# Optimization experiments

Hardware: AMD Instinct MI355X
Metric: run time of the kernel (lower is better)

## Reference

```python
import jax, jax.numpy as jnp
import numpy as np
from jax import lax

N, M, B = 512, 1024, 1024  # signal dim, atoms, batch (batch==m required by X = W @ Gamma)
POWER_ITER = 100
IHT_ITER = 50


def setup_inputs() -> dict:
    key = jax.random.key(0)
    k1, k2 = jax.random.split(key)
    Y = jax.random.normal(k1, (B, N), dtype=jnp.float32)
    W = jax.random.normal(k2, (N, M), dtype=jnp.float32)
    return {"Y": Y, "W": W, "K": 64}


def power_method(W):
    # 100 iterations of X <- X W^T W / ||.||; returns last pre-normalization norm
    # (approx largest eigenvalue of W^T W), matching PowerMethod in the source.
    X0 = jax.random.normal(jax.random.key(42), (1, W.shape[1]), dtype=W.dtype)

    def body(i, carry):
        X, _ = carry
        X2 = (X @ W.T) @ W          # [1, m]
        nm = jnp.linalg.norm(X2)
        return (X2 / nm, nm)

    _, nm = lax.fori_loop(0, POWER_ITER, body, (X0, jnp.asarray(1.0, W.dtype)))
    return nm


def hard_threshold_k(G, K):
    # keep entries strictly larger (in abs) than the (K+1)-th largest per row
    a = jnp.sort(jnp.abs(G), axis=1)[:, ::-1]   # descending per row
    T = a[:, K][:, None]                          # [B, 1]
    return G * (jnp.abs(G) > T).astype(G.dtype)


def reference(Y, W, K):
    # NormDict: column-normalize the dictionary
    W = W / jnp.linalg.norm(W, axis=0)
    c = power_method(W)
    eta = 1.0 / c
    Yn = jnp.linalg.norm(Y)

    # IHT sparse coding
    Gamma = hard_threshold_k(Y @ (eta * W), K)     # [B, m]
    residual = Gamma @ W.T - Y                      # [B, n]

    def step(carry, _):
        Gamma, residual = carry
        Gamma = hard_threshold_k(Gamma - eta * (residual @ W), K)
        residual = Gamma @ W.T - Y
        return (Gamma, residual), jnp.linalg.norm(residual) / Yn

    (Gamma, residual), norms = lax.scan(step, (Gamma, residual), None, length=IHT_ITER)

    X = W @ Gamma  # [n, m] @ [B, m] -> requires B == m, as in the torch source
    return X, Gamma, norms
```

## Files before the change

### kernel.cpp

```cpp
#include <hip/hip_runtime.h>


#define DEV __device__ __forceinline__

constexpr int Nd = 512;
constexpr int Md = 1024;
constexpr int Bd = 1024;
constexpr int Ksp = 64;
constexpr int IHT = 50;

DEV float wave_reduce_f(float v) {
#pragma unroll
  for (int off = 32; off > 0; off >>= 1) v += __shfl_down(v, off);
  return v;
}
DEV double wave_reduce_d(double v) {
#pragma unroll
  for (int off = 32; off > 0; off >>= 1) v += __shfl_down(v, off);
  return v;
}
DEV float rfl_f(float v) {
  return __uint_as_float(__builtin_amdgcn_readfirstlane(__float_as_uint(v)));
}

__global__ void k_zero(double* dacc) {
  int t = threadIdx.x;
  if (t < 51) dacc[t] = 0.0;
}

__global__ __launch_bounds__(256) void k_colnorm(const float* __restrict__ W,
                                                 float* __restrict__ cnorm) {
  int col = blockIdx.x * 256 + threadIdx.x;
  double ss = 0.0;
  for (int i = 0; i < Nd; ++i) {
    float w = W[(size_t)i * Md + col];
    ss = fma((double)w, (double)w, ss);
  }
  cnorm[col] = (float)sqrt(ss);
}

__global__ __launch_bounds__(256) void k_normalize(const float* __restrict__ W,
                                                   const float* __restrict__ cnorm,
                                                   float* __restrict__ Wn) {
  int idx = blockIdx.x * 256 + threadIdx.x;
  Wn[idx] = W[idx] / cnorm[idx & (Md - 1)];
}

__global__ __launch_bounds__(256) void k_yn2(const float* __restrict__ Y,
                                             double* __restrict__ dacc) {
  double s = 0.0;
  for (int i = blockIdx.x * 256 + threadIdx.x; i < Bd * Nd; i += gridDim.x * 256) {
    float y = Y[i];
    s = fma((double)y, (double)y, s);
  }
  s = wave_reduce_d(s);
  __shared__ double red[4];
  int lane = threadIdx.x & 63, wid = threadIdx.x >> 6;
  if (lane == 0) red[wid] = s;
  __syncthreads();
  if (threadIdx.x == 0) atomicAdd(&dacc[0], red[0] + red[1] + red[2] + red[3]);
}

template <int BM, int BN, int TN>
__global__ __launch_bounds__(256) void k_gemm_t(const float* __restrict__ A, int lda, int ta,
                                                const float* __restrict__ B, int ldb, int tb,
                                                float* __restrict__ C, int ldc, int Kd,
                                                float scale) {
  constexpr int AE = 32 * BM / 256;
  constexpr int BE = 32 * BN / 256;
  __shared__ __align__(16) float As[32][BM + 4];
  __shared__ __align__(16) float Bs[32][BN + 4];
  const int tid = threadIdx.x;
  const int tx = tid % (BN / TN), ty = tid / (BN / TN);
  const int m0 = blockIdx.y * BM, n0 = blockIdx.x * BN;
  float ra[AE], rb[BE];
  float acc[4][TN];
#pragma unroll
  for (int i = 0; i < 4; ++i)
#pragma unroll
    for (int j = 0; j < TN; ++j) acc[i][j] = 0.f;

  auto loadA = [&](int k0) {
    if (!ta) {
      const int c = tid & 31, r0 = tid >> 5;
#pragma unroll
      for (int i = 0; i < AE; ++i)
        ra[i] = A[(size_t)(m0 + r0 + i * 8) * lda + (k0 + c)];
    } else {
      const int r = tid % BM, c0 = tid / BM;
#pragma unroll
      for (int i = 0; i < AE; ++i)
        ra[i] = A[(size_t)(k0 + c0 + i * (256 / BM)) * lda + (m0 + r)];
    }
  };
  auto storeA = [&]() {
    if (!ta) {
      const int c = tid & 31, r0 = tid >> 5;
#pragma unroll
      for (int i = 0; i < AE; ++i) As[c][r0 + i * 8] = ra[i];
    } else {
      const int r = tid % BM, c0 = tid / BM;
#pragma unroll
      for (int i = 0; i < AE; ++i) As[c0 + i * (256 / BM)][r] = ra[i];
    }
  };
  auto loadB = [&](int k0) {
    if (!tb) {
      const int c = tid % BN, r0 = tid / BN;
#pragma unroll
      for (int i = 0; i < BE; ++i)
        rb[i] = B[(size_t)(k0 + r0 + i * (256 / BN)) * ldb + (n0 + c)];
    } else {
      const int r = tid & 31, c0 = tid >> 5;
#pragma unroll
      for (int i = 0; i < BE; ++i)
        rb[i] = B[(size_t)(n0 + c0 + i * 8) * ldb + (k0 + r)];
    }
  };
  auto storeB = [&]() {
    if (!tb) {
      const int c = tid % BN, r0 = tid / BN;
#pragma unroll
      for (int i = 0; i < BE; ++i) Bs[r0 + i * (256 / BN)][c] = rb[i];
    } else {
      const int r = tid & 31, c0 = tid >> 5;
#pragma unroll
      for (int i = 0; i < BE; ++i) Bs[r][c0 + i * 8] = rb[i];
    }
  };

  loadA(0);
  loadB(0);
  storeA();
  storeB();
  __syncthreads();
  for (int k0 = 0; k0 < Kd; k0 += 32) {
    const bool more = (k0 + 32) < Kd;
    if (more) { loadA(k0 + 32); loadB(k0 + 32); }
#pragma unroll
    for (int kk = 0; kk < 32; ++kk) {
      const float4 a4 = *(const float4*)&As[kk][ty * 4];
      const float aa[4] = {a4.x, a4.y, a4.z, a4.w};
      float bb[TN];
      if constexpr (TN == 4) {
        const float4 b4 = *(const float4*)&Bs[kk][tx * 4];
        bb[0] = b4.x; bb[1] = b4.y; bb[2] = b4.z; bb[3] = b4.w;
      } else {
        const float2 b2 = *(const float2*)&Bs[kk][tx * 2];
        bb[0] = b2.x; bb[1] = b2.y;
      }
#pragma unroll
      for (int i = 0; i < 4; ++i)
#pragma unroll
        for (int j = 0; j < TN; ++j) acc[i][j] = fmaf(aa[i], bb[j], acc[i][j]);
    }
    if (more) {
      __syncthreads();
      storeA();
      storeB();
      __syncthreads();
    }
  }
#pragma unroll
  for (int i = 0; i < 4; ++i) {
    if constexpr (TN == 4) {
      float4 o;
      o.x = acc[i][0] * scale; o.y = acc[i][1] * scale;
      o.z = acc[i][2] * scale; o.w = acc[i][3] * scale;
      *(float4*)&C[(size_t)(m0 + ty * 4 + i) * ldc + n0 + tx * 4] = o;
    } else {
      float2 o;
      o.x = acc[i][0] * scale; o.y = acc[i][1] * scale;
      *(float2*)&C[(size_t)(m0 + ty * 4 + i) * ldc + n0 + tx * 2] = o;
    }
  }
}

DEV float erfinv_xla(float x) {
  float w = -log1pf(-x * x);
  float p;
  if (w < 5.0f) {
    w = w - 2.5f;
    p = 2.81022636e-08f;
    p = fmaf(p, w, 3.43273939e-07f);
    p = fmaf(p, w, -3.5233877e-06f);
    p = fmaf(p, w, -4.39150654e-06f);
    p = fmaf(p, w, 0.00021858087f);
    p = fmaf(p, w, -0.00125372503f);
    p = fmaf(p, w, -0.00417768164f);
    p = fmaf(p, w, 0.246640727f);
    p = fmaf(p, w, 1.50140941f);
  } else {
    w = sqrtf(w) - 3.0f;
    p = -0.000200214257f;
    p = fmaf(p, w, 0.000100950558f);
    p = fmaf(p, w, 0.00134934322f);
    p = fmaf(p, w, -0.00367342844f);
    p = fmaf(p, w, 0.00573950773f);
    p = fmaf(p, w, -0.0076224613f);
    p = fmaf(p, w, 0.00943887047f);
    p = fmaf(p, w, 1.00167406f);
    p = fmaf(p, w, 2.83297682f);
  }
  return p * x;
}

#define TF_ROUND(r)                                  \
  {                                                  \
    x0 += x1;                                        \
    x1 = (x1 << (r)) | (x1 >> (32 - (r)));           \
    x1 ^= x0;                                        \
  }

__global__ void k_x0(float* __restrict__ X0) {
  unsigned i = threadIdx.x;
  unsigned x0 = i, x1 = i + 512u;
  const unsigned ks0 = 0u, ks1 = 42u, ks2 = 0x1BD11BDAu ^ 42u;
  x0 += ks0; x1 += ks1;
  TF_ROUND(13) TF_ROUND(15) TF_ROUND(26) TF_ROUND(6)  x0 += ks1; x1 += ks2 + 1u;
  TF_ROUND(17) TF_ROUND(29) TF_ROUND(16) TF_ROUND(24) x0 += ks2; x1 += ks0 + 2u;
  TF_ROUND(13) TF_ROUND(15) TF_ROUND(26) TF_ROUND(6)  x0 += ks0; x1 += ks1 + 3u;
  TF_ROUND(17) TF_ROUND(29) TF_ROUND(16) TF_ROUND(24) x0 += ks1; x1 += ks2 + 4u;
  TF_ROUND(13) TF_ROUND(15) TF_ROUND(26) TF_ROUND(6)  x0 += ks2; x1 += ks0 + 5u;
  const float lo = -0.99999994f;
  const float sqrt2 = 1.41421356237f;
  {
    float f = __uint_as_float((x0 >> 9) | 0x3f800000u) - 1.0f;
    float u = fmaxf(lo, f * 2.0f + lo);
    X0[i] = sqrt2 * erfinv_xla(u);
  }
  {
    float f = __uint_as_float((x1 >> 9) | 0x3f800000u) - 1.0f;
    float u = fmaxf(lo, f * 2.0f + lo);
    X0[i + 512] = sqrt2 * erfinv_xla(u);
  }
}

__global__ __launch_bounds__(256) void k_z0(const float* __restrict__ X0,
                                            const float* __restrict__ Wn,
                                            float* __restrict__ vout) {
  const int lane = threadIdx.x & 63, wid = threadIdx.x >> 6;
  const int row = blockIdx.x * 4 + wid;
  const float4* wr = (const float4*)(Wn + (size_t)row * Md);
  const float4* x4 = (const float4*)X0;
  float s = 0.f;
#pragma unroll
  for (int e = 0; e < 4; ++e) {
    const float4 w4 = wr[lane + e * 64];
    const float4 xx = x4[lane + e * 64];
    s = fmaf(w4.x, xx.x, s); s = fmaf(w4.y, xx.y, s);
    s = fmaf(w4.z, xx.z, s); s = fmaf(w4.w, xx.w, s);
  }
  s = wave_reduce_f(s);
  if (lane == 0) vout[row] = s;
}

__global__ __launch_bounds__(256) void k_pmv(const float* __restrict__ Mmat,
                                             const float* __restrict__ vin,
                                             float* __restrict__ vout, float scale) {
  const int lane = threadIdx.x & 63, wid = threadIdx.x >> 6;
  const int row = blockIdx.x * 4 + wid;
  const float4* mr = (const float4*)(Mmat + (size_t)row * Nd);
  const float4* v4 = (const float4*)vin;
  float s = 0.f;
#pragma unroll
  for (int e = 0; e < 2; ++e) {
    const float4 m4 = mr[lane + e * 64];
    const float4 xx = v4[lane + e * 64];
    s = fmaf(m4.x, xx.x, s); s = fmaf(m4.y, xx.y, s);
    s = fmaf(m4.z, xx.z, s); s = fmaf(m4.w, xx.w, s);
  }
  s = wave_reduce_f(s);
  if (lane == 0) vout[row] = s * scale;
}

__global__ __launch_bounds__(512) void k_pfinal(const float* __restrict__ v99,
                                                const float* __restrict__ v100,
                                                float* __restrict__ cbuf) {
  __shared__ double r99[8], r100[8];
  const int t = threadIdx.x, lane = t & 63, wid = t >> 6;
  double a = (double)v99[t]; a *= a;
  double b = (double)v100[t]; b *= b;
  a = wave_reduce_d(a);
  b = wave_reduce_d(b);
  if (lane == 0) { r99[wid] = a; r100[wid] = b; }
  __syncthreads();
  if (t == 0) {
    double n99 = 0.0, n100 = 0.0;
    for (int i = 0; i < 8; ++i) { n99 += r99[i]; n100 += r100[i]; }
    float c = (float)(8.0 * sqrt(n100 / n99));
    cbuf[0] = c;
    cbuf[1] = 1.0f / c;
  }
}

__global__ __launch_bounds__(256) void k_iht_all(
    const float* __restrict__ Q, const float* __restrict__ YW,
    const float* __restrict__ cbuf, float* __restrict__ gdense,
    double* __restrict__ normacc) {
  __shared__ float u[Md];
  __shared__ float yws[Md];
  __shared__ float sval[Ksp];
  __shared__ int sidx[Ksp];
  __shared__ unsigned histbuf[2][4][256];
  __shared__ unsigned wred[4];
  __shared__ unsigned sel_need, sel_prefix;
  __shared__ double dred[4];
  __shared__ int scnt;

  const int t = threadIdx.x;
  const int b = blockIdx.x;
  const int lane = t & 63, wv = t >> 6;
  const float eta = cbuf[1];
  const float4 yw = ((const float4*)(YW + (size_t)b * Md))[t];
  ((float4*)yws)[t] = yw;
#pragma unroll
  for (int e = 0; e < 8; ++e) ((unsigned*)histbuf)[t + e * 256] = 0u;
  const float* Qt = Q + t * 4;

  for (int it = -1; it < IHT; ++it) {
    if (it >= 0) {
      const int cnt = scnt;
      float4 p = make_float4(0.f, 0.f, 0.f, 0.f);
      int k = 0;
      for (; k + 8 <= cnt; k += 8) {
#define GROW(j)                                                        \
        const int id##j = __builtin_amdgcn_readfirstlane(sidx[k + j]); \
        const float g##j = rfl_f(sval[k + j]);                         \
        const float4 q##j = *(const float4*)(Qt + (size_t)id##j * Md);
        GROW(0) GROW(1) GROW(2) GROW(3) GROW(4) GROW(5) GROW(6) GROW(7)
#undef GROW
        p.x = fmaf(g0, q0.x, p.x); p.x = fmaf(g1, q1.x, p.x);
        p.x = fmaf(g2, q2.x, p.x); p.x = fmaf(g3, q3.x, p.x);
        p.x = fmaf(g4, q4.x, p.x); p.x = fmaf(g5, q5.x, p.x);
        p.x = fmaf(g6, q6.x, p.x); p.x = fmaf(g7, q7.x, p.x);
        p.y = fmaf(g0, q0.y, p.y); p.y = fmaf(g1, q1.y, p.y);
        p.y = fmaf(g2, q2.y, p.y); p.y = fmaf(g3, q3.y, p.y);
        p.y = fmaf(g4, q4.y, p.y); p.y = fmaf(g5, q5.y, p.y);
        p.y = fmaf(g6, q6.y, p.y); p.y = fmaf(g7, q7.y, p.y);
        p.z = fmaf(g0, q0.z, p.z); p.z = fmaf(g1, q1.z, p.z);
        p.z = fmaf(g2, q2.z, p.z); p.z = fmaf(g3, q3.z, p.z);
        p.z = fmaf(g4, q4.z, p.z); p.z = fmaf(g5, q5.z, p.z);
        p.z = fmaf(g6, q6.z, p.z); p.z = fmaf(g7, q7.z, p.z);
        p.w = fmaf(g0, q0.w, p.w); p.w = fmaf(g1, q1.w, p.w);
        p.w = fmaf(g2, q2.w, p.w); p.w = fmaf(g3, q3.w, p.w);
        p.w = fmaf(g4, q4.w, p.w); p.w = fmaf(g5, q5.w, p.w);
        p.w = fmaf(g6, q6.w, p.w); p.w = fmaf(g7, q7.w, p.w);
      }
      for (; k < cnt; ++k) {
        const int id = __builtin_amdgcn_readfirstlane(sidx[k]);
        const float g = rfl_f(sval[k]);
        const float4 q = *(const float4*)(Qt + (size_t)id * Md);
        p.x = fmaf(g, q.x, p.x); p.y = fmaf(g, q.y, p.y);
        p.z = fmaf(g, q.z, p.z); p.w = fmaf(g, q.w, p.w);
      }
      ((float4*)u)[t] = p;
      __syncthreads();
      if (it >= 1) {
        double part = 0.0;
        if (t < cnt) {
          const int id = sidx[t];
          part = (double)sval[t] * ((double)u[id] - 2.0 * (double)yws[id]);
        }
        part = wave_reduce_d(part);
        if (lane == 0) dred[wv] = part;
      }
      __syncthreads();
      if (it >= 1 && t == 0)
        atomicAdd(&normacc[it - 1], dred[0] + dred[1] + dred[2] + dred[3]);
      float4 uu;
      uu.x = -(eta * (p.x - yw.x)); uu.y = -(eta * (p.y - yw.y));
      uu.z = -(eta * (p.z - yw.z)); uu.w = -(eta * (p.w - yw.w));
      ((float4*)u)[t] = uu;
      __syncthreads();
      if (t < cnt) u[sidx[t]] += sval[t];
      __syncthreads();
    } else {
      float4 uu;
      uu.x = eta * yw.x; uu.y = eta * yw.y; uu.z = eta * yw.z; uu.w = eta * yw.w;
      ((float4*)u)[t] = uu;
      __syncthreads();
    }

    float vals[4];
    unsigned key[4];
    {
      const float4 mv = ((const float4*)u)[t];
      vals[0] = mv.x; vals[1] = mv.y; vals[2] = mv.z; vals[3] = mv.w;
#pragma unroll
      for (int e = 0; e < 4; ++e) key[e] = __float_as_uint(vals[e]) & 0x7fffffffu;
    }

    unsigned need = Ksp + 1, prefix = 0u, pmask = 0u;
#pragma unroll
    for (int pass = 3; pass >= 0; --pass) {
      const int sh = 8 * pass;
      const int pb = pass & 1;
      unsigned(*hist)[256] = histbuf[pb];
#pragma unroll
      for (int e = 0; e < 4; ++e)
        if ((key[e] & pmask) == prefix) atomicAdd(&hist[wv][(key[e] >> sh) & 255u], 1u);
      __syncthreads();
      unsigned* hz = histbuf[pb ^ 1][wv];
      hz[lane] = 0u; hz[lane + 64] = 0u; hz[lane + 128] = 0u; hz[lane + 192] = 0u;
      if (wv == 0) {
        const unsigned c0 = hist[0][lane] + hist[1][lane] + hist[2][lane] + hist[3][lane];
        const unsigned c1 = hist[0][lane + 64] + hist[1][lane + 64] + hist[2][lane + 64] + hist[3][lane + 64];
        const unsigned c2 = hist[0][lane + 128] + hist[1][lane + 128] + hist[2][lane + 128] + hist[3][lane + 128];
        const unsigned c3 = hist[0][lane + 192] + hist[1][lane + 192] + hist[2][lane + 192] + hist[3][lane + 192];
        unsigned s0 = c0, s1 = c1, s2 = c2, s3 = c3;
#pragma unroll
        for (int off = 1; off < 64; off <<= 1) {
          const unsigned y0 = __shfl_down(s0, off), y1 = __shfl_down(s1, off);
          const unsigned y2 = __shfl_down(s2, off), y3 = __shfl_down(s3, off);
          if (lane + off < 64) { s0 += y0; s1 += y1; s2 += y2; s3 += y3; }
        }
        const unsigned T1 = __builtin_amdgcn_readfirstlane(s1);
        const unsigned T2 = __builtin_amdgcn_readfirstlane(s2);
        const unsigned T3 = __builtin_amdgcn_readfirstlane(s3);
        const unsigned i0 = s0 + T1 + T2 + T3;
        const unsigned i1 = s1 + T2 + T3;
        const unsigned i2 = s2 + T3;
        const unsigned i3 = s3;
        if (i0 >= need && i0 - c0 < need) { sel_prefix = prefix | ((unsigned)lane << sh); sel_need = need - (i0 - c0); }
        if (i1 >= need && i1 - c1 < need) { sel_prefix = prefix | ((unsigned)(lane + 64) << sh); sel_need = need - (i1 - c1); }
        if (i2 >= need && i2 - c2 < need) { sel_prefix = prefix | ((unsigned)(lane + 128) << sh); sel_need = need - (i2 - c2); }
        if (i3 >= need && i3 - c3 < need) { sel_prefix = prefix | ((unsigned)(lane + 192) << sh); sel_need = need - (i3 - c3); }
      }
      __syncthreads();
      prefix = sel_prefix;
      need = sel_need;
      pmask |= (255u << sh);
    }
    const unsigned Tbits = prefix;

    unsigned keep = 0u;
    unsigned myc = 0u;
#pragma unroll
    for (int e = 0; e < 4; ++e)
      if (key[e] > Tbits) { keep |= (1u << e); ++myc; }
    unsigned x = myc;
#pragma unroll
    for (int off = 1; off < 64; off <<= 1) {
      const unsigned y = __shfl_up(x, off);
      if (lane >= off) x += y;
    }
    if (lane == 63) wred[wv] = x;
    __syncthreads();
    unsigned addlo = 0u;
    for (int w2 = 0; w2 < wv; ++w2) addlo += wred[w2];
    int base = (int)(x + addlo) - (int)myc;
#pragma unroll
    for (int e = 0; e < 4; ++e) {
      if (keep & (1u << e)) {
        sidx[base] = t * 4 + e;
        sval[base] = vals[e];
        ++base;
      }
    }
    if (t == 0) scnt = (int)(wred[0] + wred[1] + wred[2] + wred[3]);
    if (it == IHT - 1) {
      float4 g;
      g.x = (keep & 1u) ? vals[0] : 0.f;
      g.y = (keep & 2u) ? vals[1] : 0.f;
      g.z = (keep & 4u) ? vals[2] : 0.f;
      g.w = (keep & 8u) ? vals[3] : 0.f;
      ((float4*)(gdense + (size_t)b * Md))[t] = g;
    }
    __syncthreads();
  }

  const int cnt = scnt;
  if (wv == 0) {
    double part = 0.0;
    if (lane < cnt) {
      const int id = sidx[lane];
      float acc2 = 0.f;
      for (int k = 0; k < cnt; ++k)
        acc2 = fmaf(sval[k], Q[(size_t)sidx[k] * Md + id], acc2);
      part = (double)sval[lane] * ((double)acc2 - 2.0 * (double)yws[id]);
    }
    part = wave_reduce_d(part);
    if (lane == 0) atomicAdd(&normacc[IHT - 1], part);
  }
}

__global__ void k_wnorms(const double* __restrict__ dacc, float* __restrict__ onorms) {
  const int t = threadIdx.x;
  if (t < IHT) {
    const double yn2 = dacc[0];
    double r2 = yn2 + dacc[1 + t];
    if (r2 < 0.0) r2 = 0.0;
    onorms[t] = (float)(sqrt(r2) / sqrt(yn2));
  }
}

extern "C" void kernel_launch(void* const* d_in, const int* in_sizes, int n_in,
                              void* d_out, int out_size, void* d_ws, size_t ws_size,
                              hipStream_t stream) {
  (void)in_sizes; (void)n_in; (void)out_size; (void)ws_size;
  const float* Y = (const float*)d_in[0];
  const float* W = (const float*)d_in[1];
  float* out = (float*)d_out;
  float* outX = out;
  float* outG = out + Nd * Md;
  float* outN = outG + Bd * Md;

  char* wsb = (char*)d_ws;
  double* dacc = (double*)wsb;
  float* cbuf = (float*)(wsb + 512);
  float* Wn = (float*)(wsb + 1024);
  float* Q = Wn + Nd * Md;
  float* YW = Q + Md * Md;
  float* Smat = YW + Bd * Md;
  float* S2 = Smat + Nd * Nd;
  float* cnorm = S2 + Nd * Nd;
  float* X0 = cnorm + Md;
  float* V = X0 + Md;

  k_zero<<<1, 64, 0, stream>>>(dacc);
  k_colnorm<<<4, 256, 0, stream>>>(W, cnorm);
  k_normalize<<<2048, 256, 0, stream>>>(W, cnorm, Wn);

  k_gemm_t<64, 32, 2><<<dim3(16, 8), 256, 0, stream>>>(Wn, Md, 0, Wn, Md, 1, Smat, Nd, Md, 1.0f);
  k_gemm_t<64, 32, 2><<<dim3(16, 8), 256, 0, stream>>>(Smat, Nd, 0, Smat, Nd, 0, S2, Nd, Nd, 0.015625f);
  k_gemm_t<64, 64, 4><<<dim3(16, 16), 256, 0, stream>>>(Wn, Md, 1, Wn, Md, 0, Q, Md, Nd, 1.0f);
  k_gemm_t<64, 64, 4><<<dim3(16, 16), 256, 0, stream>>>(Y, Nd, 0, Wn, Md, 0, YW, Md, Nd, 1.0f);
  k_yn2<<<128, 256, 0, stream>>>(Y, dacc);

  k_x0<<<1, 512, 0, stream>>>(X0);
  k_z0<<<128, 256, 0, stream>>>(X0, Wn, V);
  float* pin = V;
  float* pout = V + 512;
  for (int i = 0; i < 49; ++i) {
    k_pmv<<<128, 256, 0, stream>>>(S2, pin, pout, 1.0f);
    float* tp = pin; pin = pout; pout = tp;
  }
  k_pmv<<<128, 256, 0, stream>>>(Smat, pin, V + 1024, 0.125f);
  k_pmv<<<128, 256, 0, stream>>>(Smat, V + 1024, V + 1536, 0.125f);
  k_pfinal<<<1, 512, 0, stream>>>(V + 1024, V + 1536, cbuf);

  k_iht_all<<<1024, 256, 0, stream>>>(Q, YW, cbuf, outG, dacc + 1);
  k_wnorms<<<1, 64, 0, stream>>>(dacc, outN);

  k_gemm_t<64, 32, 2><<<dim3(32, 8), 256, 0, stream>>>(Wn, Md, 0, outG, Md, 0, outX, Md, Md, 1.0f);
}
```

Baseline: 978.2 us.

## Run IHT kernel with one wavefront per batch row instead of four

Shrinks each IHT block from 256 threads to a single 64-lane wavefront. Each lane now handles 16 coefficients, so cross-wave shared-memory reductions, per-wave histograms and most block barriers go away, and the final norm step uses the whole block. The cost is less parallelism per row, more registers per lane, and more histogram atomics per lane contending on one shared histogram. With 1024 blocks of one wave each, occupancy now depends on how many blocks fit per CU rather than on block size.

```diff
diff --git a/kernel.cpp b/kernel.cpp
--- a/kernel.cpp
+++ b/kernel.cpp
@@ -294,7 +294,7 @@
   }
 }
 
-__global__ __launch_bounds__(256) void k_iht_all(
+__global__ __launch_bounds__(64) void k_iht_all(
     const float* __restrict__ Q, const float* __restrict__ YW,
     const float* __restrict__ cbuf, float* __restrict__ gdense,
     double* __restrict__ normacc) {
@@ -302,59 +302,71 @@
   __shared__ float yws[Md];
   __shared__ float sval[Ksp];
   __shared__ int sidx[Ksp];
-  __shared__ unsigned histbuf[2][4][256];
-  __shared__ unsigned wred[4];
+  __shared__ unsigned histbuf[2][256];
   __shared__ unsigned sel_need, sel_prefix;
-  __shared__ double dred[4];
   __shared__ int scnt;
 
   const int t = threadIdx.x;
   const int b = blockIdx.x;
-  const int lane = t & 63, wv = t >> 6;
   const float eta = cbuf[1];
-  const float4 yw = ((const float4*)(YW + (size_t)b * Md))[t];
-  ((float4*)yws)[t] = yw;
-#pragma unroll
-  for (int e = 0; e < 8; ++e) ((unsigned*)histbuf)[t + e * 256] = 0u;
+  const float4* YW4 = (const float4*)(YW + (size_t)b * Md);
+  float4 yw[4], p[4];
+#pragma unroll
+  for (int j = 0; j < 4; ++j) {
+    yw[j] = YW4[j * 64 + t];
+    ((float4*)yws)[j * 64 + t] = yw[j];
+  }
+  histbuf[0][t] = 0u; histbuf[0][t + 64] = 0u; histbuf[0][t + 128] = 0u; histbuf[0][t + 192] = 0u;
+  histbuf[1][t] = 0u; histbuf[1][t + 64] = 0u; histbuf[1][t + 128] = 0u; histbuf[1][t + 192] = 0u;
   const float* Qt = Q + t * 4;
 
   for (int it = -1; it < IHT; ++it) {
+    float vals[16];
+    unsigned key[16];
     if (it >= 0) {
       const int cnt = scnt;
-      float4 p = make_float4(0.f, 0.f, 0.f, 0.f);
+#pragma unroll
+      for (int j = 0; j < 4; ++j) p[j] = make_float4(0.f, 0.f, 0.f, 0.f);
       int k = 0;
-      for (; k + 8 <= cnt; k += 8) {
-#define GROW(j)                                                        \
-        const int id##j = __builtin_amdgcn_readfirstlane(sidx[k + j]); \
-        const float g##j = rfl_f(sval[k + j]);                         \
-        const float4 q##j = *(const float4*)(Qt + (size_t)id##j * Md);
-        GROW(0) GROW(1) GROW(2) GROW(3) GROW(4) GROW(5) GROW(6) GROW(7)
-#undef GROW
-        p.x = fmaf(g0, q0.x, p.x); p.x = fmaf(g1, q1.x, p.x);
-        p.x = fmaf(g2, q2.x, p.x); p.x = fmaf(g3, q3.x, p.x);
-        p.x = fmaf(g4, q4.x, p.x); p.x = fmaf(g5, q5.x, p.x);
-        p.x = fmaf(g6, q6.x, p.x); p.x = fmaf(g7, q7.x, p.x);
-        p.y = fmaf(g0, q0.y, p.y); p.y = fmaf(g1, q1.y, p.y);
-        p.y = fmaf(g2, q2.y, p.y); p.y = fmaf(g3, q3.y, p.y);
-        p.y = fmaf(g4, q4.y, p.y); p.y = fmaf(g5, q5.y, p.y);
-        p.y = fmaf(g6, q6.y, p.y); p.y = fmaf(g7, q7.y, p.y);
-        p.z = fmaf(g0, q0.z, p.z); p.z = fmaf(g1, q1.z, p.z);
-        p.z = fmaf(g2, q2.z, p.z); p.z = fmaf(g3, q3.z, p.z);
-        p.z = fmaf(g4, q4.z, p.z); p.z = fmaf(g5, q5.z, p.z);
-        p.z = fmaf(g6, q6.z, p.z); p.z = fmaf(g7, q7.z, p.z);
-        p.w = fmaf(g0, q0.w, p.w); p.w = fmaf(g1, q1.w, p.w);
-        p.w = fmaf(g2, q2.w, p.w); p.w = fmaf(g3, q3.w, p.w);
-        p.w = fmaf(g4, q4.w, p.w); p.w = fmaf(g5, q5.w, p.w);
-        p.w = fmaf(g6, q6.w, p.w); p.w = fmaf(g7, q7.w, p.w);
+      for (; k + 4 <= cnt; k += 4) {
+        const int i0 = __builtin_amdgcn_readfirstlane(sidx[k]);
+        const int i1 = __builtin_amdgcn_readfirstlane(sidx[k + 1]);
+        const int i2 = __builtin_amdgcn_readfirstlane(sidx[k + 2]);
+        const int i3 = __builtin_amdgcn_readfirstlane(sidx[k + 3]);
+        const float g0 = rfl_f(sval[k]), g1 = rfl_f(sval[k + 1]);
+        const float g2 = rfl_f(sval[k + 2]), g3 = rfl_f(sval[k + 3]);
+        float4 q0[4], q1[4], q2[4], q3[4];
+#pragma unroll
+        for (int j = 0; j < 4; ++j) {
+          q0[j] = *(const float4*)(Qt + (size_t)i0 * Md + j * 256);
+          q1[j] = *(const float4*)(Qt + (size_t)i1 * Md + j * 256);
+          q2[j] = *(const float4*)(Qt + (size_t)i2 * Md + j * 256);
+          q3[j] = *(const float4*)(Qt + (size_t)i3 * Md + j * 256);
+        }
+#pragma unroll
+        for (int j = 0; j < 4; ++j) {
+          p[j].x = fmaf(g0, q0[j].x, p[j].x); p[j].x = fmaf(g1, q1[j].x, p[j].x);
+          p[j].x = fmaf(g2, q2[j].x, p[j].x); p[j].x = fmaf(g3, q3[j].x, p[j].x);
+          p[j].y = fmaf(g0, q0[j].y, p[j].y); p[j].y = fmaf(g1, q1[j].y, p[j].y);
+          p[j].y = fmaf(g2, q2[j].y, p[j].y); p[j].y = fmaf(g3, q3[j].y, p[j].y);
+          p[j].z = fmaf(g0, q0[j].z, p[j].z); p[j].z = fmaf(g1, q1[j].z, p[j].z);
+          p[j].z = fmaf(g2, q2[j].z, p[j].z); p[j].z = fmaf(g3, q3[j].z, p[j].z);
+          p[j].w = fmaf(g0, q0[j].w, p[j].w); p[j].w = fmaf(g1, q1[j].w, p[j].w);
+          p[j].w = fmaf(g2, q2[j].w, p[j].w); p[j].w = fmaf(g3, q3[j].w, p[j].w);
+        }
       }
       for (; k < cnt; ++k) {
         const int id = __builtin_amdgcn_readfirstlane(sidx[k]);
         const float g = rfl_f(sval[k]);
-        const float4 q = *(const float4*)(Qt + (size_t)id * Md);
-        p.x = fmaf(g, q.x, p.x); p.y = fmaf(g, q.y, p.y);
-        p.z = fmaf(g, q.z, p.z); p.w = fmaf(g, q.w, p.w);
-      }
-      ((float4*)u)[t] = p;
+#pragma unroll
+        for (int j = 0; j < 4; ++j) {
+          const float4 q = *(const float4*)(Qt + (size_t)id * Md + j * 256);
+          p[j].x = fmaf(g, q.x, p[j].x); p[j].y = fmaf(g, q.y, p[j].y);
+          p[j].z = fmaf(g, q.z, p[j].z); p[j].w = fmaf(g, q.w, p[j].w);
+        }
+      }
+#pragma unroll
+      for (int j = 0; j < 4; ++j) ((float4*)u)[j * 64 + t] = p[j];
       __syncthreads();
       if (it >= 1) {
         double part = 0.0;
@@ -363,70 +375,67 @@
           part = (double)sval[t] * ((double)u[id] - 2.0 * (double)yws[id]);
         }
         part = wave_reduce_d(part);
-        if (lane == 0) dred[wv] = part;
-      }
-      __syncthreads();
-      if (it >= 1 && t == 0)
-        atomicAdd(&normacc[it - 1], dred[0] + dred[1] + dred[2] + dred[3]);
-      float4 uu;
-      uu.x = -(eta * (p.x - yw.x)); uu.y = -(eta * (p.y - yw.y));
-      uu.z = -(eta * (p.z - yw.z)); uu.w = -(eta * (p.w - yw.w));
-      ((float4*)u)[t] = uu;
+        if (t == 0) atomicAdd(&normacc[it - 1], part);
+      }
+      __syncthreads();
+#pragma unroll
+      for (int j = 0; j < 4; ++j) {
+        float4 uu;
+        uu.x = -(eta * (p[j].x - yw[j].x)); uu.y = -(eta * (p[j].y - yw[j].y));
+        uu.z = -(eta * (p[j].z - yw[j].z)); uu.w = -(eta * (p[j].w - yw[j].w));
+        ((float4*)u)[j * 64 + t] = uu;
+      }
       __syncthreads();
       if (t < cnt) u[sidx[t]] += sval[t];
       __syncthreads();
+#pragma unroll
+      for (int j = 0; j < 4; ++j) {
+        const float4 mv = ((const float4*)u)[j * 64 + t];
+        vals[j * 4 + 0] = mv.x; vals[j * 4 + 1] = mv.y;
+        vals[j * 4 + 2] = mv.z; vals[j * 4 + 3] = mv.w;
+      }
     } else {
-      float4 uu;
-      uu.x = eta * yw.x; uu.y = eta * yw.y; uu.z = eta * yw.z; uu.w = eta * yw.w;
-      ((float4*)u)[t] = uu;
-      __syncthreads();
-    }
-
-    float vals[4];
-    unsigned key[4];
-    {
-      const float4 mv = ((const float4*)u)[t];
-      vals[0] = mv.x; vals[1] = mv.y; vals[2] = mv.z; vals[3] = mv.w;
-#pragma unroll
-      for (int e = 0; e < 4; ++e) key[e] = __float_as_uint(vals[e]) & 0x7fffffffu;
-    }
+#pragma unroll
+      for (int j = 0; j < 4; ++j) {
+        vals[j * 4 + 0] = eta * yw[j].x; vals[j * 4 + 1] = eta * yw[j].y;
+        vals[j * 4 + 2] = eta * yw[j].z; vals[j * 4 + 3] = eta * yw[j].w;
+      }
+    }
+#pragma unroll
+    for (int e = 0; e < 16; ++e) key[e] = __float_as_uint(vals[e]) & 0x7fffffffu;
 
     unsigned need = Ksp + 1, prefix = 0u, pmask = 0u;
 #pragma unroll
     for (int pass = 3; pass >= 0; --pass) {
       const int sh = 8 * pass;
       const int pb = pass & 1;
-      unsigned(*hist)[256] = histbuf[pb];
-#pragma unroll
-      for (int e = 0; e < 4; ++e)
-        if ((key[e] & pmask) == prefix) atomicAdd(&hist[wv][(key[e] >> sh) & 255u], 1u);
-      __syncthreads();
-      unsigned* hz = histbuf[pb ^ 1][wv];
-      hz[lane] = 0u; hz[lane + 64] = 0u; hz[lane + 128] = 0u; hz[lane + 192] = 0u;
-      if (wv == 0) {
-        const unsigned c0 = hist[0][lane] + hist[1][lane] + hist[2][lane] + hist[3][lane];
-        const unsigned c1 = hist[0][lane + 64] + hist[1][lane + 64] + hist[2][lane + 64] + hist[3][lane + 64];
-        const unsigned c2 = hist[0][lane + 128] + hist[1][lane + 128] + hist[2][lane + 128] + hist[3][lane + 128];
-        const unsigned c3 = hist[0][lane + 192] + hist[1][lane + 192] + hist[2][lane + 192] + hist[3][lane + 192];
-        unsigned s0 = c0, s1 = c1, s2 = c2, s3 = c3;
-#pragma unroll
-        for (int off = 1; off < 64; off <<= 1) {
-          const unsigned y0 = __shfl_down(s0, off), y1 = __shfl_down(s1, off);
-          const unsigned y2 = __shfl_down(s2, off), y3 = __shfl_down(s3, off);
-          if (lane + off < 64) { s0 += y0; s1 += y1; s2 += y2; s3 += y3; }
-        }
-        const unsigned T1 = __builtin_amdgcn_readfirstlane(s1);
-        const unsigned T2 = __builtin_amdgcn_readfirstlane(s2);
-        const unsigned T3 = __builtin_amdgcn_readfirstlane(s3);
-        const unsigned i0 = s0 + T1 + T2 + T3;
-        const unsigned i1 = s1 + T2 + T3;
-        const unsigned i2 = s2 + T3;
-        const unsigned i3 = s3;
-        if (i0 >= need && i0 - c0 < need) { sel_prefix = prefix | ((unsigned)lane << sh); sel_need = need - (i0 - c0); }
-        if (i1 >= need && i1 - c1 < need) { sel_prefix = prefix | ((unsigned)(lane + 64) << sh); sel_need = need - (i1 - c1); }
-        if (i2 >= need && i2 - c2 < need) { sel_prefix = prefix | ((unsigned)(lane + 128) << sh); sel_need = need - (i2 - c2); }
-        if (i3 >= need && i3 - c3 < need) { sel_prefix = prefix | ((unsigned)(lane + 192) << sh); sel_need = need - (i3 - c3); }
-      }
+      unsigned* hist = histbuf[pb];
+#pragma unroll
+      for (int e = 0; e < 16; ++e)
+        if ((key[e] & pmask) == prefix) atomicAdd(&hist[(key[e] >> sh) & 255u], 1u);
+      __syncthreads();
+      unsigned* hz = histbuf[pb ^ 1];
+      hz[t] = 0u; hz[t + 64] = 0u; hz[t + 128] = 0u; hz[t + 192] = 0u;
+      const unsigned c0 = hist[t], c1 = hist[t + 64];
+      const unsigned c2 = hist[t + 128], c3 = hist[t + 192];
+      unsigned s0 = c0, s1 = c1, s2 = c2, s3 = c3;
+#pragma unroll
+      for (int off = 1; off < 64; off <<= 1) {
+        const unsigned y0 = __shfl_down(s0, off), y1 = __shfl_down(s1, off);
+        const unsigned y2 = __shfl_down(s2, off), y3 = __shfl_down(s3, off);
+        if (t + off < 64) { s0 += y0; s1 += y1; s2 += y2; s3 += y3; }
+      }
+      const unsigned T1 = __builtin_amdgcn_readfirstlane(s1);
+      const unsigned T2 = __builtin_amdgcn_readfirstlane(s2);
+      const unsigned T3 = __builtin_amdgcn_readfirstlane(s3);
+      const unsigned i0 = s0 + T1 + T2 + T3;
+      const unsigned i1 = s1 + T2 + T3;
+      const unsigned i2 = s2 + T3;
+      const unsigned i3 = s3;
+      if (i0 >= need && i0 - c0 < need) { sel_prefix = prefix | ((unsigned)t << sh); sel_need = need - (i0 - c0); }
+      if (i1 >= need && i1 - c1 < need) { sel_prefix = prefix | ((unsigned)(t + 64) << sh); sel_need = need - (i1 - c1); }
+      if (i2 >= need && i2 - c2 < need) { sel_prefix = prefix | ((unsigned)(t + 128) << sh); sel_need = need - (i2 - c2); }
+      if (i3 >= need && i3 - c3 < need) { sel_prefix = prefix | ((unsigned)(t + 192) << sh); sel_need = need - (i3 - c3); }
       __syncthreads();
       prefix = sel_prefix;
       need = sel_need;
@@ -435,54 +444,67 @@
     const unsigned Tbits = prefix;
 
     unsigned keep = 0u;
-    unsigned myc = 0u;
-#pragma unroll
-    for (int e = 0; e < 4; ++e)
-      if (key[e] > Tbits) { keep |= (1u << e); ++myc; }
-    unsigned x = myc;
-#pragma unroll
-    for (int off = 1; off < 64; off <<= 1) {
-      const unsigned y = __shfl_up(x, off);
-      if (lane >= off) x += y;
-    }
-    if (lane == 63) wred[wv] = x;
+    int mycj[4];
+#pragma unroll
+    for (int j = 0; j < 4; ++j) {
+      int c = 0;
+#pragma unroll
+      for (int e = 0; e < 4; ++e)
+        if (key[j * 4 + e] > Tbits) { keep |= (1u << (j * 4 + e)); ++c; }
+      mycj[j] = c;
+    }
+    int basej[4];
+    int total = 0;
+#pragma unroll
+    for (int j = 0; j < 4; ++j) {
+      int x = mycj[j];
+#pragma unroll
+      for (int off = 1; off < 64; off <<= 1) {
+        const int y = __shfl_up(x, off);
+        if (t >= off) x += y;
+      }
+      basej[j] = total + x - mycj[j];
+      total += __shfl(x, 63);
+    }
+#pragma unroll
+    for (int j = 0; j < 4; ++j) {
+      int base = basej[j];
+#pragma unroll
+      for (int e = 0; e < 4; ++e) {
+        if (keep & (1u << (j * 4 + e))) {
+          sidx[base] = j * 256 + 4 * t + e;
+          sval[base] = vals[j * 4 + e];
+          ++base;
+        }
+      }
+    }
+    if (t == 0) scnt = total;
+    if (it == IHT - 1) {
+      float4* G4 = (float4*)(gdense + (size_t)b * Md);
+#pragma unroll
+      for (int j = 0; j < 4; ++j) {
+        float4 g;
+        g.x = (keep & (1u << (j * 4 + 0))) ? vals[j * 4 + 0] : 0.f;
+        g.y = (keep & (1u << (j * 4 + 1))) ? vals[j * 4 + 1] : 0.f;
+        g.z = (keep & (1u << (j * 4 + 2))) ? vals[j * 4 + 2] : 0.f;
+        g.w = (keep & (1u << (j * 4 + 3))) ? vals[j * 4 + 3] : 0.f;
+        G4[j * 64 + t] = g;
+      }
+    }
     __syncthreads();
-    unsigned addlo = 0u;
-    for (int w2 = 0; w2 < wv; ++w2) addlo += wred[w2];
-    int base = (int)(x + addlo) - (int)myc;
-#pragma unroll
-    for (int e = 0; e < 4; ++e) {
-      if (keep & (1u << e)) {
-        sidx[base] = t * 4 + e;
-        sval[base] = vals[e];
-        ++base;
-      }
-    }
-    if (t == 0) scnt = (int)(wred[0] + wred[1] + wred[2] + wred[3]);
-    if (it == IHT - 1) {
-      float4 g;
-      g.x = (keep & 1u) ? vals[0] : 0.f;
-      g.y = (keep & 2u) ? vals[1] : 0.f;
-      g.z = (keep & 4u) ? vals[2] : 0.f;
-      g.w = (keep & 8u) ? vals[3] : 0.f;
-      ((float4*)(gdense + (size_t)b * Md))[t] = g;
-    }
-    __syncthreads();
   }
 
   const int cnt = scnt;
-  if (wv == 0) {
-    double part = 0.0;
-    if (lane < cnt) {
-      const int id = sidx[lane];
-      float acc2 = 0.f;
-      for (int k = 0; k < cnt; ++k)
-        acc2 = fmaf(sval[k], Q[(size_t)sidx[k] * Md + id], acc2);
-      part = (double)sval[lane] * ((double)acc2 - 2.0 * (double)yws[id]);
-    }
-    part = wave_reduce_d(part);
-    if (lane == 0) atomicAdd(&normacc[IHT - 1], part);
-  }
+  double part = 0.0;
+  if (t < cnt) {
+    const int id = sidx[t];
+    float acc2 = 0.f;
+    for (int k = 0; k < cnt; ++k)
+      acc2 = fmaf(sval[k], Q[(size_t)sidx[k] * Md + id], acc2);
+    part = (double)sval[t] * ((double)acc2 - 2.0 * (double)yws[id]);
+  }
+  part = wave_reduce_d(part);
+  if (t == 0) atomicAdd(&normacc[IHT - 1], part);
 }
 
 __global__ void k_wnorms(const double* __restrict__ dacc, float* __restrict__ onorms) {
@@ -540,7 +562,7 @@
   k_pmv<<<128, 256, 0, stream>>>(Smat, V + 1024, V + 1536, 0.125f);
   k_pfinal<<<1, 512, 0, stream>>>(V + 1024, V + 1536, cbuf);
 
-  k_iht_all<<<1024, 256, 0, stream>>>(Q, YW, cbuf, outG, dacc + 1);
+  k_iht_all<<<1024, 64, 0, stream>>>(Q, YW, cbuf, outG, dacc + 1);
   k_wnorms<<<1, 64, 0, stream>>>(dacc, outN);
 
   k_gemm_t<64, 32, 2><<<dim3(32, 8), 256, 0, stream>>>(Wn, Md, 0, outG, Md, 0, outX, Md, Md, 1.0f);
```

After: 1.204 ms. +23.0%, slower.

## Fuse power-method launches into one persistent kernel with grid barriers

Applied to the files above, without the earlier changes.

Replaces the ~54 small launches of the power method (x0 generation, z0, 51 matvecs, final norm) with a single 8-block persistent kernel. The blocks synchronise between matvec steps through per-step atomic counters in global memory, which are zeroed by k_zero. This removes per-launch overhead and gaps between dependent tiny kernels, but only 8 workgroups do the matvecs and the spin barriers add latency. The IHT gather loop is also widened from 8 to 16 rows per batch, and k_iht_all gets a launch-bounds occupancy hint of 4.

```diff
diff --git a/kernel.cpp b/kernel.cpp
--- a/kernel.cpp
+++ b/kernel.cpp
@@ -23,9 +23,10 @@
   return __uint_as_float(__builtin_amdgcn_readfirstlane(__float_as_uint(v)));
 }
 
-__global__ void k_zero(double* dacc) {
+__global__ void k_zero(double* dacc, int* pcnt) {
   int t = threadIdx.x;
   if (t < 51) dacc[t] = 0.0;
+  if (t < 52) pcnt[t] = 0;
 }
 
 __global__ __launch_bounds__(256) void k_colnorm(const float* __restrict__ W,
@@ -212,89 +213,121 @@
     x1 ^= x0;                                        \
   }
 
-__global__ void k_x0(float* __restrict__ X0) {
-  unsigned i = threadIdx.x;
-  unsigned x0 = i, x1 = i + 512u;
-  const unsigned ks0 = 0u, ks1 = 42u, ks2 = 0x1BD11BDAu ^ 42u;
-  x0 += ks0; x1 += ks1;
-  TF_ROUND(13) TF_ROUND(15) TF_ROUND(26) TF_ROUND(6)  x0 += ks1; x1 += ks2 + 1u;
-  TF_ROUND(17) TF_ROUND(29) TF_ROUND(16) TF_ROUND(24) x0 += ks2; x1 += ks0 + 2u;
-  TF_ROUND(13) TF_ROUND(15) TF_ROUND(26) TF_ROUND(6)  x0 += ks0; x1 += ks1 + 3u;
-  TF_ROUND(17) TF_ROUND(29) TF_ROUND(16) TF_ROUND(24) x0 += ks1; x1 += ks2 + 4u;
-  TF_ROUND(13) TF_ROUND(15) TF_ROUND(26) TF_ROUND(6)  x0 += ks2; x1 += ks0 + 5u;
-  const float lo = -0.99999994f;
-  const float sqrt2 = 1.41421356237f;
+__global__ __launch_bounds__(512) void k_power(const float* __restrict__ Wn,
+                                               const float* __restrict__ S2,
+                                               const float* __restrict__ Smat,
+                                               float* __restrict__ V,
+                                               float* __restrict__ cbuf,
+                                               int* __restrict__ pcnt) {
+  __shared__ float xbuf[Md];
+  __shared__ double r99[8], r100[8];
+  const int t = threadIdx.x, lane = t & 63, wv = t >> 6;
+  const int bk = blockIdx.x;
+  const int nblk = (int)gridDim.x;
+
   {
-    float f = __uint_as_float((x0 >> 9) | 0x3f800000u) - 1.0f;
-    float u = fmaxf(lo, f * 2.0f + lo);
-    X0[i] = sqrt2 * erfinv_xla(u);
-  }
-  {
-    float f = __uint_as_float((x1 >> 9) | 0x3f800000u) - 1.0f;
-    float u = fmaxf(lo, f * 2.0f + lo);
-    X0[i + 512] = sqrt2 * erfinv_xla(u);
-  }
-}
-
-__global__ __launch_bounds__(256) void k_z0(const float* __restrict__ X0,
-                                            const float* __restrict__ Wn,
-                                            float* __restrict__ vout) {
-  const int lane = threadIdx.x & 63, wid = threadIdx.x >> 6;
-  const int row = blockIdx.x * 4 + wid;
-  const float4* wr = (const float4*)(Wn + (size_t)row * Md);
-  const float4* x4 = (const float4*)X0;
-  float s = 0.f;
-#pragma unroll
-  for (int e = 0; e < 4; ++e) {
-    const float4 w4 = wr[lane + e * 64];
-    const float4 xx = x4[lane + e * 64];
-    s = fmaf(w4.x, xx.x, s); s = fmaf(w4.y, xx.y, s);
-    s = fmaf(w4.z, xx.z, s); s = fmaf(w4.w, xx.w, s);
-  }
-  s = wave_reduce_f(s);
-  if (lane == 0) vout[row] = s;
-}
-
-__global__ __launch_bounds__(256) void k_pmv(const float* __restrict__ Mmat,
-                                             const float* __restrict__ vin,
-                                             float* __restrict__ vout, float scale) {
-  const int lane = threadIdx.x & 63, wid = threadIdx.x >> 6;
-  const int row = blockIdx.x * 4 + wid;
-  const float4* mr = (const float4*)(Mmat + (size_t)row * Nd);
-  const float4* v4 = (const float4*)vin;
-  float s = 0.f;
-#pragma unroll
-  for (int e = 0; e < 2; ++e) {
-    const float4 m4 = mr[lane + e * 64];
-    const float4 xx = v4[lane + e * 64];
-    s = fmaf(m4.x, xx.x, s); s = fmaf(m4.y, xx.y, s);
-    s = fmaf(m4.z, xx.z, s); s = fmaf(m4.w, xx.w, s);
-  }
-  s = wave_reduce_f(s);
-  if (lane == 0) vout[row] = s * scale;
-}
-
-__global__ __launch_bounds__(512) void k_pfinal(const float* __restrict__ v99,
-                                                const float* __restrict__ v100,
-                                                float* __restrict__ cbuf) {
-  __shared__ double r99[8], r100[8];
-  const int t = threadIdx.x, lane = t & 63, wid = t >> 6;
-  double a = (double)v99[t]; a *= a;
-  double b = (double)v100[t]; b *= b;
-  a = wave_reduce_d(a);
-  b = wave_reduce_d(b);
-  if (lane == 0) { r99[wid] = a; r100[wid] = b; }
+    unsigned i = (unsigned)t;
+    unsigned x0 = i, x1 = i + 512u;
+    const unsigned ks0 = 0u, ks1 = 42u, ks2 = 0x1BD11BDAu ^ 42u;
+    x0 += ks0; x1 += ks1;
+    TF_ROUND(13) TF_ROUND(15) TF_ROUND(26) TF_ROUND(6)  x0 += ks1; x1 += ks2 + 1u;
+    TF_ROUND(17) TF_ROUND(29) TF_ROUND(16) TF_ROUND(24) x0 += ks2; x1 += ks0 + 2u;
+    TF_ROUND(13) TF_ROUND(15) TF_ROUND(26) TF_ROUND(6)  x0 += ks0; x1 += ks1 + 3u;
+    TF_ROUND(17) TF_ROUND(29) TF_ROUND(16) TF_ROUND(24) x0 += ks1; x1 += ks2 + 4u;
+    TF_ROUND(13) TF_ROUND(15) TF_ROUND(26) TF_ROUND(6)  x0 += ks2; x1 += ks0 + 5u;
+    const float lo = -0.99999994f;
+    const float sqrt2 = 1.41421356237f;
+    {
+      float f = __uint_as_float((x0 >> 9) | 0x3f800000u) - 1.0f;
+      float u = fmaxf(lo, f * 2.0f + lo);
+      xbuf[i] = sqrt2 * erfinv_xla(u);
+    }
+    {
+      float f = __uint_as_float((x1 >> 9) | 0x3f800000u) - 1.0f;
+      float u = fmaxf(lo, f * 2.0f + lo);
+      xbuf[i + 512] = sqrt2 * erfinv_xla(u);
+    }
+  }
+  __syncthreads();
+
+  float* s0 = V;
+  float* s1 = V + 512;
+  float* v99 = V + 1024;
+  float* v100 = V + 1536;
+  const int w = bk * 8 + wv;
+
+  for (int i = 0; i < 8; ++i) {
+    const int row = w + 64 * i;
+    const float4* wr = (const float4*)(Wn + (size_t)row * Md);
+    const float4* x4 = (const float4*)xbuf;
+    float s = 0.f;
+#pragma unroll
+    for (int e = 0; e < 4; ++e) {
+      const float4 w4 = wr[lane + e * 64];
+      const float4 xx = x4[lane + e * 64];
+      s = fmaf(w4.x, xx.x, s); s = fmaf(w4.y, xx.y, s);
+      s = fmaf(w4.z, xx.z, s); s = fmaf(w4.w, xx.w, s);
+    }
+    s = wave_reduce_f(s);
+    if (lane == 0) s0[row] = s;
+  }
   __syncthreads();
   if (t == 0) {
-    double n99 = 0.0, n100 = 0.0;
-    for (int i = 0; i < 8; ++i) { n99 += r99[i]; n100 += r100[i]; }
-    float c = (float)(8.0 * sqrt(n100 / n99));
-    cbuf[0] = c;
-    cbuf[1] = 1.0f / c;
-  }
-}
-
-__global__ __launch_bounds__(256) void k_iht_all(
+    __hip_atomic_fetch_add(&pcnt[0], 1, __ATOMIC_RELEASE, __HIP_MEMORY_SCOPE_AGENT);
+    while (__hip_atomic_load(&pcnt[0], __ATOMIC_ACQUIRE, __HIP_MEMORY_SCOPE_AGENT) < nblk) {}
+  }
+  __syncthreads();
+
+  const float* pin = s0;
+  for (int step = 0; step < 51; ++step) {
+    const float* M;
+    float scale;
+    float* dst;
+    if (step < 49)      { M = S2;   scale = 1.0f;   dst = (step & 1) ? s0 : s1; }
+    else if (step == 49){ M = Smat; scale = 0.125f; dst = v99; }
+    else                { M = Smat; scale = 0.125f; dst = v100; }
+    for (int i = 0; i < 8; ++i) {
+      const int row = w + 64 * i;
+      const float4* mr = (const float4*)(M + (size_t)row * Nd);
+      const float4* v4 = (const float4*)pin;
+      float s = 0.f;
+#pragma unroll
+      for (int e = 0; e < 2; ++e) {
+        const float4 m4 = mr[lane + e * 64];
+        const float4 xx = v4[lane + e * 64];
+        s = fmaf(m4.x, xx.x, s); s = fmaf(m4.y, xx.y, s);
+        s = fmaf(m4.z, xx.z, s); s = fmaf(m4.w, xx.w, s);
+      }
+      s = wave_reduce_f(s);
+      if (lane == 0) dst[row] = s * scale;
+    }
+    __syncthreads();
+    if (t == 0) {
+      __hip_atomic_fetch_add(&pcnt[1 + step], 1, __ATOMIC_RELEASE, __HIP_MEMORY_SCOPE_AGENT);
+      while (__hip_atomic_load(&pcnt[1 + step], __ATOMIC_ACQUIRE, __HIP_MEMORY_SCOPE_AGENT) < nblk) {}
+    }
+    __syncthreads();
+    pin = dst;
+  }
+
+  if (bk == 0) {
+    double a = (double)v99[t]; a *= a;
+    double b2 = (double)v100[t]; b2 *= b2;
+    a = wave_reduce_d(a);
+    b2 = wave_reduce_d(b2);
+    if (lane == 0) { r99[wv] = a; r100[wv] = b2; }
+    __syncthreads();
+    if (t == 0) {
+      double n99 = 0.0, n100 = 0.0;
+      for (int i = 0; i < 8; ++i) { n99 += r99[i]; n100 += r100[i]; }
+      float c = (float)(8.0 * sqrt(n100 / n99));
+      cbuf[0] = c;
+      cbuf[1] = 1.0f / c;
+    }
+  }
+}
+
+__global__ __launch_bounds__(256, 4) void k_iht_all(
     const float* __restrict__ Q, const float* __restrict__ YW,
     const float* __restrict__ cbuf, float* __restrict__ gdense,
     double* __restrict__ normacc) {
@@ -323,29 +356,25 @@
       const int cnt = scnt;
       float4 p = make_float4(0.f, 0.f, 0.f, 0.f);
       int k = 0;
-      for (; k + 8 <= cnt; k += 8) {
-#define GROW(j)                                                        \
-        const int id##j = __builtin_amdgcn_readfirstlane(sidx[k + j]); \
-        const float g##j = rfl_f(sval[k + j]);                         \
-        const float4 q##j = *(const float4*)(Qt + (size_t)id##j * Md);
-        GROW(0) GROW(1) GROW(2) GROW(3) GROW(4) GROW(5) GROW(6) GROW(7)
-#undef GROW
-        p.x = fmaf(g0, q0.x, p.x); p.x = fmaf(g1, q1.x, p.x);
-        p.x = fmaf(g2, q2.x, p.x); p.x = fmaf(g3, q3.x, p.x);
-        p.x = fmaf(g4, q4.x, p.x); p.x = fmaf(g5, q5.x, p.x);
-        p.x = fmaf(g6, q6.x, p.x); p.x = fmaf(g7, q7.x, p.x);
-        p.y = fmaf(g0, q0.y, p.y); p.y = fmaf(g1, q1.y, p.y);
-        p.y = fmaf(g2, q2.y, p.y); p.y = fmaf(g3, q3.y, p.y);
-        p.y = fmaf(g4, q4.y, p.y); p.y = fmaf(g5, q5.y, p.y);
-        p.y = fmaf(g6, q6.y, p.y); p.y = fmaf(g7, q7.y, p.y);
-        p.z = fmaf(g0, q0.z, p.z); p.z = fmaf(g1, q1.z, p.z);
-        p.z = fmaf(g2, q2.z, p.z); p.z = fmaf(g3, q3.z, p.z);
-        p.z = fmaf(g4, q4.z, p.z); p.z = fmaf(g5, q5.z, p.z);
-        p.z = fmaf(g6, q6.z, p.z); p.z = fmaf(g7, q7.z, p.z);
-        p.w = fmaf(g0, q0.w, p.w); p.w = fmaf(g1, q1.w, p.w);
-        p.w = fmaf(g2, q2.w, p.w); p.w = fmaf(g3, q3.w, p.w);
-        p.w = fmaf(g4, q4.w, p.w); p.w = fmaf(g5, q5.w, p.w);
-        p.w = fmaf(g6, q6.w, p.w); p.w = fmaf(g7, q7.w, p.w);
+      for (; k + 16 <= cnt; k += 16) {
+        int ids[16];
+        float gs[16];
+        float4 qq[16];
+#pragma unroll
+        for (int j = 0; j < 16; ++j) {
+          ids[j] = __builtin_amdgcn_readfirstlane(sidx[k + j]);
+          gs[j] = rfl_f(sval[k + j]);
+        }
+#pragma unroll
+        for (int j = 0; j < 16; ++j) qq[j] = *(const float4*)(Qt + (size_t)ids[j] * Md);
+#pragma unroll
+        for (int j = 0; j < 16; ++j) p.x = fmaf(gs[j], qq[j].x, p.x);
+#pragma unroll
+        for (int j = 0; j < 16; ++j) p.y = fmaf(gs[j], qq[j].y, p.y);
+#pragma unroll
+        for (int j = 0; j < 16; ++j) p.z = fmaf(gs[j], qq[j].z, p.z);
+#pragma unroll
+        for (int j = 0; j < 16; ++j) p.w = fmaf(gs[j], qq[j].w, p.w);
       }
       for (; k < cnt; ++k) {
         const int id = __builtin_amdgcn_readfirstlane(sidx[k]);
@@ -515,10 +544,10 @@
   float* Smat = YW + Bd * Md;
   float* S2 = Smat + Nd * Nd;
   float* cnorm = S2 + Nd * Nd;
-  float* X0 = cnorm + Md;
-  float* V = X0 + Md;
-
-  k_zero<<<1, 64, 0, stream>>>(dacc);
+  float* V = cnorm + Md;
+  int* pcnt = (int*)(V + 2048);
+
+  k_zero<<<1, 64, 0, stream>>>(dacc, pcnt);
   k_colnorm<<<4, 256, 0, stream>>>(W, cnorm);
   k_normalize<<<2048, 256, 0, stream>>>(W, cnorm, Wn);
 
@@ -528,17 +557,7 @@
   k_gemm_t<64, 64, 4><<<dim3(16, 16), 256, 0, stream>>>(Y, Nd, 0, Wn, Md, 0, YW, Md, Nd, 1.0f);
   k_yn2<<<128, 256, 0, stream>>>(Y, dacc);
 
-  k_x0<<<1, 512, 0, stream>>>(X0);
-  k_z0<<<128, 256, 0, stream>>>(X0, Wn, V);
-  float* pin = V;
-  float* pout = V + 512;
-  for (int i = 0; i < 49; ++i) {
-    k_pmv<<<128, 256, 0, stream>>>(S2, pin, pout, 1.0f);
-    float* tp = pin; pin = pout; pout = tp;
-  }
-  k_pmv<<<128, 256, 0, stream>>>(Smat, pin, V + 1024, 0.125f);
-  k_pmv<<<128, 256, 0, stream>>>(Smat, V + 1024, V + 1536, 0.125f);
-  k_pfinal<<<1, 512, 0, stream>>>(V + 1024, V + 1536, cbuf);
+  k_power<<<8, 512, 0, stream>>>(Wn, S2, Smat, V, cbuf, pcnt);
 
   k_iht_all<<<1024, 256, 0, stream>>>(Q, YW, cbuf, outG, dacc + 1);
   k_wnorms<<<1, 64, 0, stream>>>(dacc, outN);
```

After: 1.066 ms. 1.09x slower.
